# Kernel tuning notes

Measured on AMD Instinct MI355X. Metric: run time of the kernel, lower is better.

## Reference

```python
import jax, jax.numpy as jnp
import numpy as np

HEADS = 8
REL_MAX = 64  # module-level constant REL_MAX_DIST


def _to_c(x):
    # x: [..., 2] real/imag interleaved (torch.view_as_real layout) -> complex
    return jax.lax.complex(x[..., 0], x[..., 1])


def setup_inputs() -> dict:
    key = jax.random.key(0)
    ks = jax.random.split(key, 12)
    dim, past_len = 256, 65536
    d2 = dim * 2
    s = 1.0 / np.sqrt(d2)  # torch Linear default init range

    def lin(k):
        kw, kb = jax.random.split(k)
        W = jax.random.uniform(kw, (d2, d2), jnp.float32, -s, s)
        b = jax.random.uniform(kb, (d2,), jnp.float32, -s, s)
        return W, b

    Wq, bq = lin(ks[0])
    Wk, bk = lin(ks[1])
    Wv, bv = lin(ks[2])
    Wo, bo = lin(ks[3])
    return {
        "curr_pos": past_len,
        "z_curr": jax.random.normal(ks[4], (dim, 2), jnp.float32),
        "z_past": jax.random.normal(ks[5], (past_len, dim, 2), jnp.float32),
        "Wq": Wq, "bq": bq, "Wk": Wk, "bk": bk,
        "Wv": Wv, "bv": bv, "Wo": Wo, "bo": bo,
        "rel_bias": jax.random.normal(ks[6], (2 * REL_MAX + 1, dim, 2), jnp.float32) * 0.02,
    }


def reference(curr_pos, z_curr, z_past, Wq, bq, Wk, bk, Wv, bv, Wo, bo, rel_bias):
    dim = z_curr.shape[0]
    past_len = z_past.shape[0]
    head_dim = dim // HEADS

    # real-valued linear projections on interleaved (real, imag) features
    q_proj = z_curr.reshape(-1) @ Wq.T + bq                        # [2*dim]
    k_proj = z_past.reshape(past_len, -1) @ Wk.T + bk              # [L, 2*dim]
    v_proj = z_past.reshape(past_len, -1) @ Wv.T + bv              # [L, 2*dim]

    # view as complex, split heads
    q_h = _to_c(q_proj.reshape(dim, 2)).reshape(HEADS, head_dim)               # [H, hd]
    k_h = _to_c(k_proj.reshape(past_len, dim, 2)).reshape(past_len, HEADS, head_dim)
    v_h = _to_c(v_proj.reshape(past_len, dim, 2)).reshape(past_len, HEADS, head_dim)

    # Re(<q, k>) per head
    dot_scores = jnp.real(jnp.conj(q_h)[None] * k_h).sum(-1)       # [L, H]

    # relative positional bias (gather + clamp)
    rel_dists = jnp.arange(curr_pos - past_len, curr_pos)
    idx = jnp.clip(rel_dists + REL_MAX, 0, 2 * REL_MAX)
    rb_h = _to_c(rel_bias)[idx].reshape(past_len, HEADS, head_dim)
    rel_scores = jnp.real(jnp.conj(q_h)[None] * rb_h).sum(-1)      # [L, H]

    scores = (dot_scores + rel_scores) / np.sqrt(head_dim)
    weights = jax.nn.softmax(scores, axis=0)                       # softmax over past_len

    out_h = (weights[..., None] * v_h).sum(0)                      # [H, hd] complex
    out_c = out_h.reshape(dim)
    out_real = jnp.stack([jnp.real(out_c), jnp.imag(out_c)], -1).reshape(-1)  # [2*dim]
    out = out_real @ Wo.T + bo
    # return real view [dim, 2] of the complex output (view_as_complex layout)
    return out.reshape(dim, 2)
```

## Files before the change

kernel.cpp:

```cpp
#include <hip/hip_runtime.h>
#include <math.h>


static constexpr float SCALE = 0.17677669529663687f;

__device__ __forceinline__ float wave_sum(float v) {
#pragma unroll
  for (int off = 32; off > 0; off >>= 1) v += __shfl_xor(v, off, 64);
  return v;
}

__global__ __launch_bounds__(256) void k_matvec512(
    const float* __restrict__ M, const float* __restrict__ x,
    const float* __restrict__ bias, float* __restrict__ y) {
  const int wave = threadIdx.x >> 6, lane = threadIdx.x & 63;
  const int j = blockIdx.x * 4 + wave;
  const float* Mr = M + (size_t)j * 512 + lane * 8;
  const float4 m0 = *(const float4*)Mr;
  const float4 m1 = *(const float4*)(Mr + 4);
  const float4 x0 = *(const float4*)(x + lane * 8);
  const float4 x1 = *(const float4*)(x + lane * 8 + 4);
  float acc = m0.x * x0.x + m0.y * x0.y + m0.z * x0.z + m0.w * x0.w +
              m1.x * x1.x + m1.y * x1.y + m1.z * x1.z + m1.w * x1.w;
  acc = wave_sum(acc);
  if (lane == 0) y[j] = acc + bias[j];
}

__global__ __launch_bounds__(256) void k_wkpart(
    const float* __restrict__ Wk, const float* __restrict__ qp,
    float* __restrict__ wkpart) {
  __shared__ float ql[32];
  const int b = blockIdx.x;
  if (threadIdx.x < 32) ql[threadIdx.x] = qp[b * 32 + threadIdx.x];
  __syncthreads();
  for (int i = threadIdx.x; i < 512; i += 256) {
    float acc = 0.f;
#pragma unroll
    for (int k = 0; k < 32; ++k)
      acc += ql[k] * Wk[(size_t)(b * 32 + k) * 512 + i];
    wkpart[b * 512 + i] = acc;
  }
}

__global__ __launch_bounds__(256) void k_misc(
    const float* __restrict__ qp, const float* __restrict__ bk,
    const float* __restrict__ rb, const float* __restrict__ wkpart,
    float* __restrict__ wk, float* __restrict__ ck, float* __restrict__ relq,
    float* __restrict__ S_un) {
  const int b = blockIdx.x;
  if (b < 8) {
    for (int i = threadIdx.x; i < 512; i += 256)
      wk[b * 512 + i] =
          (wkpart[(2 * b) * 512 + i] + wkpart[(2 * b + 1) * 512 + i]) * SCALE;
  } else if (b == 8) {
    if (threadIdx.x < 8) {
      const int h = threadIdx.x;
      float acc = 0.f;
      for (int k = 0; k < 64; ++k) acc += qp[h * 64 + k] * bk[h * 64 + k];
      ck[h] = acc * SCALE;
    }
  } else if (b < 14) {
    const int t = (b - 9) * 256 + threadIdx.x;
    if (t < 129 * 8) {
      const int idx = t >> 3, h = t & 7;
      float acc = 0.f;
      for (int k = 0; k < 64; ++k)
        acc += qp[h * 64 + k] * rb[(size_t)idx * 512 + h * 64 + k];
      relq[t] = acc * SCALE;
    }
  } else {
    for (int t = threadIdx.x; t < 4096; t += 256) S_un[t] = 0.f;
  }
}

__global__ __launch_bounds__(256, 2) void k_attn(
    const float* __restrict__ zp, const float* __restrict__ wk,
    const float* __restrict__ ck, const float* __restrict__ relq,
    const int* __restrict__ curr_pos, int L, float* __restrict__ Sp,
    float* __restrict__ sp) {
  __shared__ float relql[1032];
  __shared__ float Sl[4096];
  __shared__ float sl[4][8];
  const int tid = threadIdx.x;
  const int wave = tid >> 6, lane = tid & 63;
  for (int t = tid; t < 1032; t += 256) relql[t] = relq[t];

  float wkr[8][8];
#pragma unroll
  for (int h = 0; h < 8; ++h) {
    const float4 a = *(const float4*)(wk + h * 512 + lane * 8);
    const float4 b = *(const float4*)(wk + h * 512 + lane * 8 + 4);
    wkr[h][0] = a.x; wkr[h][1] = a.y; wkr[h][2] = a.z; wkr[h][3] = a.w;
    wkr[h][4] = b.x; wkr[h][5] = b.y; wkr[h][6] = b.z; wkr[h][7] = b.w;
  }
  const int myh = ((lane & 1) << 2) | (lane & 2) | ((lane >> 2) & 1);
  const float ck_my = ck[myh];
  const int cp = curr_pos[0];
  __syncthreads();

  float S[8][8];
#pragma unroll
  for (int h = 0; h < 8; ++h)
#pragma unroll
    for (int k = 0; k < 8; ++k) S[h][k] = 0.f;
  float s_loc = 0.f;

  const int l0 = blockIdx.x * 128 + wave * 32;
  const float* zr = zp + (size_t)l0 * 512 + lane * 8;
  float4 p0 = *(const float4*)zr;
  float4 p1 = *(const float4*)(zr + 4);

#pragma unroll 2
  for (int r = 0; r < 32; ++r) {
    const int l = l0 + r;
    const float* zn = (l + 1 < L) ? (zr + 512) : zr;
    const float4 n0 = *(const float4*)zn;
    const float4 n1 = *(const float4*)(zn + 4);
    const float zz[8] = {p0.x, p0.y, p0.z, p0.w, p1.x, p1.y, p1.z, p1.w};
    float acc[8];
#pragma unroll
    for (int h = 0; h < 8; ++h) {
      float a = 0.f;
#pragma unroll
      for (int k = 0; k < 8; ++k) a += zz[k] * wkr[h][k];
      acc[h] = a;
    }
    const bool lo1 = (lane & 1) == 0;
    float b0 = (lo1 ? acc[0] : acc[4]) + __shfl_xor(lo1 ? acc[4] : acc[0], 1, 64);
    float b1 = (lo1 ? acc[1] : acc[5]) + __shfl_xor(lo1 ? acc[5] : acc[1], 1, 64);
    float b2 = (lo1 ? acc[2] : acc[6]) + __shfl_xor(lo1 ? acc[6] : acc[2], 1, 64);
    float b3 = (lo1 ? acc[3] : acc[7]) + __shfl_xor(lo1 ? acc[7] : acc[3], 1, 64);
    const bool lo2 = (lane & 2) == 0;
    float c0 = (lo2 ? b0 : b2) + __shfl_xor(lo2 ? b2 : b0, 2, 64);
    float c1 = (lo2 ? b1 : b3) + __shfl_xor(lo2 ? b3 : b1, 2, 64);
    const bool lo3 = (lane & 4) == 0;
    float d = (lo3 ? c0 : c1) + __shfl_xor(lo3 ? c1 : c0, 4, 64);
    d += __shfl_xor(d, 8, 64);
    d += __shfl_xor(d, 16, 64);
    d += __shfl_xor(d, 32, 64);

    int dd = cp - L + l + 64;
    dd = dd < 0 ? 0 : (dd > 128 ? 128 : dd);
    float w = __expf(d + ck_my + relql[dd * 8 + myh]);
    if (l >= L) w = 0.f;
    s_loc += w;
#pragma unroll
    for (int h = 0; h < 8; ++h) {
      const int src = ((h & 1) << 2) | (h & 2) | ((h >> 2) & 1);
      const float wh = __shfl(w, src, 64);
#pragma unroll
      for (int k = 0; k < 8; ++k) S[h][k] += wh * zz[k];
    }
    p0 = n0; p1 = n1; zr += 512;
  }

  if (lane < 8) sl[wave][myh] = s_loc;
  for (int wv = 0; wv < 4; ++wv) {
    if (wave == wv) {
#pragma unroll
      for (int h = 0; h < 8; ++h)
#pragma unroll
        for (int k = 0; k < 8; ++k) {
          const int idx = h * 512 + lane * 8 + k;
          if (wv == 0) Sl[idx] = S[h][k];
          else Sl[idx] += S[h][k];
        }
    }
    __syncthreads();
  }
  for (int t = tid; t < 4096; t += 256)
    Sp[(size_t)blockIdx.x * 4096 + t] = Sl[t];
  if (tid < 8)
    sp[blockIdx.x * 8 + tid] = sl[0][tid] + sl[1][tid] + sl[2][tid] + sl[3][tid];
}

__global__ __launch_bounds__(256) void k_comb2(
    const float* __restrict__ Sp, const float* __restrict__ spv, int nb,
    float* __restrict__ S_un, float* __restrict__ s) {
  if (blockIdx.x < 256) {
    const int T = blockIdx.x * 256 + threadIdx.x;
    const int col = T & 4095;
    const int g = T >> 12;
    const int chunk = (nb + 15) >> 4;
    const int r0 = g * chunk;
    const int r1 = min(r0 + chunk, nb);
    float a[8];
#pragma unroll
    for (int u = 0; u < 8; ++u) a[u] = 0.f;
    int b = r0;
    for (; b + 8 <= r1; b += 8) {
#pragma unroll
      for (int u = 0; u < 8; ++u) a[u] += Sp[(size_t)(b + u) * 4096 + col];
    }
    for (; b < r1; ++b) a[0] += Sp[(size_t)b * 4096 + col];
    const float t = ((a[0] + a[1]) + (a[2] + a[3])) +
                    ((a[4] + a[5]) + (a[6] + a[7]));
    atomicAdd(&S_un[col], t);
  } else {
    __shared__ float red[256];
    float a = 0.f;
    for (int b2 = threadIdx.x >> 3; b2 < nb; b2 += 32)
      a += spv[b2 * 8 + (threadIdx.x & 7)];
    red[threadIdx.x] = a;
    __syncthreads();
    if (threadIdx.x < 8) {
      float x = 0.f;
      for (int c = 0; c < 32; ++c) x += red[c * 8 + threadIdx.x];
      s[threadIdx.x] = x;
    }
  }
}

__global__ __launch_bounds__(256) void k_outreal(
    const float* __restrict__ Wv, const float* __restrict__ S_un,
    const float* __restrict__ s, const float* __restrict__ bv,
    float* __restrict__ out_real) {
  const int wave = threadIdx.x >> 6, lane = threadIdx.x & 63;
  const int j = blockIdx.x * 4 + wave;
  const int h = j >> 6;
  const float* Mr = Wv + (size_t)j * 512 + lane * 8;
  const float* xr = S_un + h * 512 + lane * 8;
  const float4 m0 = *(const float4*)Mr;
  const float4 m1 = *(const float4*)(Mr + 4);
  const float4 x0 = *(const float4*)xr;
  const float4 x1 = *(const float4*)(xr + 4);
  float acc = m0.x * x0.x + m0.y * x0.y + m0.z * x0.z + m0.w * x0.w +
              m1.x * x1.x + m1.y * x1.y + m1.z * x1.z + m1.w * x1.w;
  acc = wave_sum(acc);
  if (lane == 0) out_real[j] = acc / s[h] + bv[j];
}

extern "C" void kernel_launch(void* const* d_in, const int* in_sizes, int n_in,
                              void* d_out, int out_size, void* d_ws,
                              size_t ws_size, hipStream_t stream) {
  const int* curr_pos = (const int*)d_in[0];
  const float* z_curr = (const float*)d_in[1];
  const float* z_past = (const float*)d_in[2];
  const float* Wq = (const float*)d_in[3];
  const float* bq = (const float*)d_in[4];
  const float* Wk = (const float*)d_in[5];
  const float* bk = (const float*)d_in[6];
  const float* Wv = (const float*)d_in[7];
  const float* bv = (const float*)d_in[8];
  const float* Wo = (const float*)d_in[9];
  const float* bo = (const float*)d_in[10];
  const float* rb = (const float*)d_in[11];
  float* out = (float*)d_out;

  const int L = in_sizes[2] / 512;
  const int nb = (L + 127) / 128;

  float* ws = (float*)d_ws;
  size_t o = 0;
  float* qp = ws + o;       o += 512;
  float* wkpart = ws + o;   o += 16 * 512;
  float* wk = ws + o;       o += 8 * 512;
  float* ck = ws + o;       o += 16;
  float* relq = ws + o;     o += 1040;
  float* s = ws + o;        o += 8;
  float* sp = ws + o;       o += (size_t)nb * 8;
  float* S_un = ws + o;     o += 4096;
  float* out_real = ws + o; o += 512;
  float* Sp = ws + o;       o += (size_t)nb * 4096;
  (void)ws_size; (void)n_in; (void)out_size;

  k_matvec512<<<128, 256, 0, stream>>>(Wq, z_curr, bq, qp);
  k_wkpart<<<16, 256, 0, stream>>>(Wk, qp, wkpart);
  k_misc<<<15, 256, 0, stream>>>(qp, bk, rb, wkpart, wk, ck, relq, S_un);
  k_attn<<<nb, 256, 0, stream>>>(z_past, wk, ck, relq, curr_pos, L, Sp, sp);
  k_comb2<<<257, 256, 0, stream>>>(Sp, sp, nb, S_un, s);
  k_outreal<<<128, 256, 0, stream>>>(Wv, S_un, s, bv, out_real);
  k_matvec512<<<128, 256, 0, stream>>>(Wo, out_real, bo, out);
}
```

Measured before the change: 244.0 us.

## Fuse q projection and per-head precompute into one front kernel; two-row prefetch in attention

```diff
diff --git a/kernel.cpp b/kernel.cpp
--- a/kernel.cpp
+++ b/kernel.cpp
@@ -26,50 +26,52 @@
   if (lane == 0) y[j] = acc + bias[j];
 }
 
-__global__ __launch_bounds__(256) void k_wkpart(
-    const float* __restrict__ Wk, const float* __restrict__ qp,
-    float* __restrict__ wkpart) {
-  __shared__ float ql[32];
-  const int b = blockIdx.x;
-  if (threadIdx.x < 32) ql[threadIdx.x] = qp[b * 32 + threadIdx.x];
-  __syncthreads();
-  for (int i = threadIdx.x; i < 512; i += 256) {
-    float acc = 0.f;
-#pragma unroll
-    for (int k = 0; k < 32; ++k)
-      acc += ql[k] * Wk[(size_t)(b * 32 + k) * 512 + i];
-    wkpart[b * 512 + i] = acc;
-  }
-}
-
-__global__ __launch_bounds__(256) void k_misc(
-    const float* __restrict__ qp, const float* __restrict__ bk,
-    const float* __restrict__ rb, const float* __restrict__ wkpart,
+__global__ __launch_bounds__(256) void k_front(
+    const float* __restrict__ Wq, const float* __restrict__ bq,
+    const float* __restrict__ zc, const float* __restrict__ Wk,
+    const float* __restrict__ bk, const float* __restrict__ rb,
     float* __restrict__ wk, float* __restrict__ ck, float* __restrict__ relq,
     float* __restrict__ S_un) {
+  __shared__ float ql[64];
   const int b = blockIdx.x;
+  const int h = b & 7;
+  const int wave = threadIdx.x >> 6, lane = threadIdx.x & 63;
+  const float4 x0 = *(const float4*)(zc + lane * 8);
+  const float4 x1 = *(const float4*)(zc + lane * 8 + 4);
+  for (int rr = 0; rr < 16; ++rr) {
+    const int j = h * 64 + wave * 16 + rr;
+    const float* Mr = Wq + (size_t)j * 512 + lane * 8;
+    const float4 m0 = *(const float4*)Mr;
+    const float4 m1 = *(const float4*)(Mr + 4);
+    float acc = m0.x * x0.x + m0.y * x0.y + m0.z * x0.z + m0.w * x0.w +
+                m1.x * x1.x + m1.y * x1.y + m1.z * x1.z + m1.w * x1.w;
+    acc = wave_sum(acc);
+    if (lane == 0) ql[wave * 16 + rr] = acc + bq[j];
+  }
+  __syncthreads();
   if (b < 8) {
-    for (int i = threadIdx.x; i < 512; i += 256)
-      wk[b * 512 + i] =
-          (wkpart[(2 * b) * 512 + i] + wkpart[(2 * b + 1) * 512 + i]) * SCALE;
-  } else if (b == 8) {
-    if (threadIdx.x < 8) {
-      const int h = threadIdx.x;
+    if (wave == 0) {
+      float acc = ql[lane] * bk[h * 64 + lane];
+      acc = wave_sum(acc);
+      if (lane == 0) ck[h] = acc * SCALE;
+    }
+    for (int i = threadIdx.x; i < 512; i += 256) {
       float acc = 0.f;
-      for (int k = 0; k < 64; ++k) acc += qp[h * 64 + k] * bk[h * 64 + k];
-      ck[h] = acc * SCALE;
-    }
-  } else if (b < 14) {
-    const int t = (b - 9) * 256 + threadIdx.x;
-    if (t < 129 * 8) {
-      const int idx = t >> 3, h = t & 7;
+#pragma unroll
+      for (int k = 0; k < 64; ++k)
+        acc += ql[k] * Wk[(size_t)(h * 64 + k) * 512 + i];
+      wk[h * 512 + i] = acc * SCALE;
+      S_un[h * 512 + i] = 0.f;
+    }
+  } else {
+    const int t = threadIdx.x;
+    if (t < 129) {
       float acc = 0.f;
+#pragma unroll
       for (int k = 0; k < 64; ++k)
-        acc += qp[h * 64 + k] * rb[(size_t)idx * 512 + h * 64 + k];
-      relq[t] = acc * SCALE;
-    }
-  } else {
-    for (int t = threadIdx.x; t < 4096; t += 256) S_un[t] = 0.f;
+        acc += ql[k] * rb[(size_t)t * 512 + h * 64 + k];
+      relq[t * 8 + h] = acc * SCALE;
+    }
   }
 }
 
@@ -106,17 +108,15 @@
   float s_loc = 0.f;
 
   const int l0 = blockIdx.x * 128 + wave * 32;
-  const float* zr = zp + (size_t)l0 * 512 + lane * 8;
-  float4 p0 = *(const float4*)zr;
-  float4 p1 = *(const float4*)(zr + 4);
-
-#pragma unroll 2
-  for (int r = 0; r < 32; ++r) {
-    const int l = l0 + r;
-    const float* zn = (l + 1 < L) ? (zr + 512) : zr;
-    const float4 n0 = *(const float4*)zn;
-    const float4 n1 = *(const float4*)(zn + 4);
-    const float zz[8] = {p0.x, p0.y, p0.z, p0.w, p1.x, p1.y, p1.z, p1.w};
+  const size_t lmax = (size_t)(L - 1);
+  auto rowptr = [&](int l) {
+    size_t ll = (size_t)l;
+    if (ll > lmax) ll = lmax;
+    return zp + ll * 512 + lane * 8;
+  };
+
+  auto process = [&](const float4& z0, const float4& z1, int l) {
+    const float zz[8] = {z0.x, z0.y, z0.z, z0.w, z1.x, z1.y, z1.z, z1.w};
     float acc[8];
 #pragma unroll
     for (int h = 0; h < 8; ++h) {
@@ -151,7 +151,25 @@
 #pragma unroll
       for (int k = 0; k < 8; ++k) S[h][k] += wh * zz[k];
     }
-    p0 = n0; p1 = n1; zr += 512;
+  };
+
+  const float* r0 = rowptr(l0);
+  const float* r1 = rowptr(l0 + 1);
+  float4 a0 = *(const float4*)r0;
+  float4 a1 = *(const float4*)(r0 + 4);
+  float4 b0 = *(const float4*)r1;
+  float4 b1 = *(const float4*)(r1 + 4);
+
+  for (int r = 0; r < 32; r += 2) {
+    const float* rn0 = rowptr(l0 + r + 2);
+    const float* rn1 = rowptr(l0 + r + 3);
+    const float4 c0 = *(const float4*)rn0;
+    const float4 c1 = *(const float4*)(rn0 + 4);
+    const float4 d0 = *(const float4*)rn1;
+    const float4 d1 = *(const float4*)(rn1 + 4);
+    process(a0, a1, l0 + r);
+    process(b0, b1, l0 + r + 1);
+    a0 = c0; a1 = c1; b0 = d0; b1 = d1;
   }
 
   if (lane < 8) sl[wave][myh] = s_loc;
@@ -252,8 +270,6 @@
 
   float* ws = (float*)d_ws;
   size_t o = 0;
-  float* qp = ws + o;       o += 512;
-  float* wkpart = ws + o;   o += 16 * 512;
   float* wk = ws + o;       o += 8 * 512;
   float* ck = ws + o;       o += 16;
   float* relq = ws + o;     o += 1040;
@@ -264,9 +280,8 @@
   float* Sp = ws + o;       o += (size_t)nb * 4096;
   (void)ws_size; (void)n_in; (void)out_size;
 
-  k_matvec512<<<128, 256, 0, stream>>>(Wq, z_curr, bq, qp);
-  k_wkpart<<<16, 256, 0, stream>>>(Wk, qp, wkpart);
-  k_misc<<<15, 256, 0, stream>>>(qp, bk, rb, wkpart, wk, ck, relq, S_un);
+  k_front<<<16, 256, 0, stream>>>(Wq, bq, z_curr, Wk, bk, rb, wk, ck, relq,
+                                  S_un);
   k_attn<<<nb, 256, 0, stream>>>(z_past, wk, ck, relq, curr_pos, L, Sp, sp);
   k_comb2<<<257, 256, 0, stream>>>(Sp, sp, nb, S_un, s);
   k_outreal<<<128, 256, 0, stream>>>(Wv, S_un, s, bv, out_real);
```

Result: slower. 288.0 us (+18.0%).
